# Kernel tuning notes

Hardware: AMD Instinct MI355X
Metric: run time of the kernel (lower is better)

## Reference

```python
import jax, jax.numpy as jnp
import numpy as np

N_NODES = 100000
N_EDGES = 3200000
F_IN = 512
F_OUT = 512
T_ITERS = 4
EPS = 1e-5


def setup_inputs() -> dict:
    key = jax.random.key(0)
    k1, k2, k3, k4, k5 = jax.random.split(key, 5)
    x = jax.random.normal(k1, (N_NODES, F_IN), dtype=jnp.float32)
    stdv = 1.0 / np.sqrt(F_OUT)
    weight = jax.random.uniform(k2, (F_IN, F_OUT), dtype=jnp.float32,
                                minval=-stdv, maxval=stdv)
    adj_rows = jax.random.randint(k3, (N_EDGES,), 0, N_NODES, dtype=jnp.int32)
    adj_cols = jax.random.randint(k4, (N_EDGES,), 0, N_NODES, dtype=jnp.int32)
    adj_vals = jax.random.uniform(k5, (N_EDGES,), dtype=jnp.float32)
    return {"x": x, "weight": weight, "adj_rows": adj_rows,
            "adj_cols": adj_cols, "adj_vals": adj_vals}


def oni_norm(weight):
    # norm_groups=1: Z is [in_features, out_features]
    Zc = weight - weight.mean(axis=-1, keepdims=True)
    S = Zc @ Zc.T + EPS * jnp.eye(Zc.shape[0], dtype=weight.dtype)
    norm_S = jnp.linalg.norm(S)  # Frobenius norm (scalar)
    S = S / norm_S
    B = jnp.eye(S.shape[-1], dtype=weight.dtype)
    for _ in range(T_ITERS):
        # baddbmm(1.5, B, -0.5, B^3, S) = 1.5*B - 0.5*(B@B@B)@S
        B3 = B @ B @ B
        B = 1.5 * B - 0.5 * (B3 @ S)
    W = (B @ Zc) / jnp.sqrt(norm_S)
    return W


def reference(x, weight, adj_rows, adj_cols, adj_vals):
    # Faithful to the torch forward: ONINorm(W) is computed (self.W) but the
    # dense mm uses the raw self.weight, exactly as in the source.
    W = oni_norm(weight)  # noqa: F841 (computed but unused, as in original)
    support = x @ weight                       # [N, F_OUT]
    # spmm: out[r] = sum_e adj_vals[e] * support[cols[e]] for rows[e] == r
    gathered = adj_vals[:, None] * support[adj_cols]  # [E, F_OUT]
    output = jax.ops.segment_sum(gathered, adj_rows, num_segments=N_NODES)
    return output
```

## Files before the change

kernel.cpp:

```cpp
#include <hip/hip_runtime.h>
#include <hip/hip_bf16.h>

#define N_NODESC 100000
#define N_EDGESC 3200000
#define FDIM 512
#define MPAD 100096
#define NBLK 256
#define EPB 12500
#define NBUCKB 391
#define NCNT (NBLK * NBUCKB)
#define NB_SCAN ((NCNT + 8191) / 8192)

typedef __attribute__((ext_vector_type(4))) float f32x4;
typedef __attribute__((ext_vector_type(8))) __bf16 bf16x8;
typedef __attribute__((ext_vector_type(4))) __bf16 bf16x4;
typedef unsigned long long u64;

__device__ __forceinline__ void gload_lds16(const void* g, void* l) {
  __builtin_amdgcn_global_load_lds(
      (const __attribute__((address_space(1))) unsigned int*)g,
      (__attribute__((address_space(3))) unsigned int*)l, 16, 0, 0);
}

__global__ void k_convert_wT(const float* __restrict__ w, __bf16* __restrict__ wT) {
  int i = blockIdx.x * 256 + threadIdx.x;
  if (i >= FDIM * FDIM) return;
  int k = i >> 9, n = i & (FDIM - 1);
  wT[n * FDIM + k] = (__bf16)w[i];
}

__global__ __launch_bounds__(256) void k_bcount(const int* __restrict__ rows,
                                                int* __restrict__ cnt) {
  __shared__ int h[NBUCKB];
  const int blk = blockIdx.x;
  for (int i = threadIdx.x; i < NBUCKB; i += 256) h[i] = 0;
  __syncthreads();
  const int e0 = blk * EPB;
  for (int e = e0 + threadIdx.x; e < e0 + EPB; e += 256)
    atomicAdd(&h[rows[e] >> 8], 1);
  __syncthreads();
  for (int i = threadIdx.x; i < NBUCKB; i += 256) cnt[i * NBLK + blk] = h[i];
}

__global__ __launch_bounds__(1024) void k_scan1(int* __restrict__ d, int* __restrict__ bsum) {
  __shared__ int s[1024];
  const int t = threadIdx.x;
  const int base = blockIdx.x * 8192 + t * 8;
  int v[8];
  int sum = 0;
  #pragma unroll
  for (int k = 0; k < 8; ++k) {
    v[k] = (base + k < NCNT) ? d[base + k] : 0;
    sum += v[k];
  }
  s[t] = sum;
  __syncthreads();
  for (int dl = 1; dl < 1024; dl <<= 1) {
    int a = s[t];
    int b = (t >= dl) ? s[t - dl] : 0;
    __syncthreads();
    s[t] = a + b;
    __syncthreads();
  }
  int excl = (t == 0) ? 0 : s[t - 1];
  #pragma unroll
  for (int k = 0; k < 8; ++k) {
    if (base + k < NCNT) d[base + k] = excl;
    excl += v[k];
  }
  if (t == 1023) bsum[blockIdx.x] = s[1023];
}

__global__ __launch_bounds__(1024) void k_scan2(int* __restrict__ bsum, int nb,
                                                int* __restrict__ d) {
  __shared__ int s[1024];
  const int t = threadIdx.x;
  s[t] = (t < nb) ? bsum[t] : 0;
  __syncthreads();
  for (int dl = 1; dl < 1024; dl <<= 1) {
    int a = s[t];
    int b = (t >= dl) ? s[t - dl] : 0;
    __syncthreads();
    s[t] = a + b;
    __syncthreads();
  }
  if (t < nb) bsum[t] = (t == 0) ? 0 : s[t - 1];
  if (t == 0) d[NCNT] = s[1023];
}

__global__ void k_scan3(int* __restrict__ d, const int* __restrict__ bsum) {
  int i = blockIdx.x * 256 + threadIdx.x;
  if (i >= NCNT) return;
  d[i] += bsum[i >> 13];
}

__global__ __launch_bounds__(256) void k_bscatter(const int* __restrict__ rows,
                                                  const int* __restrict__ cols,
                                                  const float* __restrict__ vals,
                                                  const int* __restrict__ off,
                                                  u64* __restrict__ bedges) {
  __shared__ int lofs[NBUCKB];
  __shared__ int lcur[NBUCKB];
  const int blk = blockIdx.x;
  for (int i = threadIdx.x; i < NBUCKB; i += 256) {
    lofs[i] = off[i * NBLK + blk];
    lcur[i] = 0;
  }
  __syncthreads();
  const int e0 = blk * EPB;
  for (int e = e0 + threadIdx.x; e < e0 + EPB; e += 256) {
    const int r = rows[e];
    const int b = r >> 8;
    const int p = lofs[b] + atomicAdd(&lcur[b], 1);
    bedges[p] = ((u64)__float_as_uint(vals[e]) << 32) |
                ((u64)(r & 255) << 17) | (unsigned)cols[e];
  }
}

__global__ __launch_bounds__(256) void k_csr(const int* __restrict__ off,
                                             const u64* __restrict__ bedges,
                                             u64* __restrict__ edges,
                                             int* __restrict__ row_off) {
  __shared__ int hcnt[256];
  __shared__ int hcur[256];
  const int b = blockIdx.x;
  const int t = threadIdx.x;
  const int base  = off[b * NBLK];
  const int nextb = (b + 1 < NBUCKB) ? off[(b + 1) * NBLK] : off[NCNT];
  hcnt[t] = 0;
  __syncthreads();
  for (int j = base + t; j < nextb; j += 256)
    atomicAdd(&hcnt[(int)(bedges[j] >> 17) & 255], 1);
  __syncthreads();
  for (int d = 1; d < 256; d <<= 1) {
    int a = hcnt[t];
    int u = (t >= d) ? hcnt[t - d] : 0;
    __syncthreads();
    hcnt[t] = a + u;
    __syncthreads();
  }
  const int excl = (t == 0) ? 0 : hcnt[t - 1];
  row_off[b * 256 + t] = base + excl;
  hcur[t] = base + excl;
  __syncthreads();
  for (int j = base + t; j < nextb; j += 256) {
    const u64 e = bedges[j];
    const int lr = (int)(e >> 17) & 255;
    const int p = atomicAdd(&hcur[lr], 1);
    edges[p] = (e & 0xFFFFFFFF00000000ull) | (e & 0x1FFFFull);
  }
}

__global__ __launch_bounds__(512) void k_gemm(const float* __restrict__ x,
                                              const __bf16* __restrict__ wT,
                                              __bf16* __restrict__ support) {
  __shared__ __bf16 lA[2][256 * 32];
  __shared__ __bf16 lB[2][256 * 32];
  const int tm = blockIdx.x >> 1;
  const int tn = blockIdx.x & 1;
  const int tid = threadIdx.x;
  const int wid = tid >> 6;
  const int lane = tid & 63;
  const int wm = wid >> 2;
  const int wn = wid & 3;

  const long rowA0 = (long)tm * 256;
  const int  ncol0 = tn * 256;

  const int srow  = lane >> 2;
  const int skoff = (lane & 3) * 8;

  const int arow = tid >> 1;
  const int ah   = (tid & 1) * 16;

  f32x4 acc[8][4];
  #pragma unroll
  for (int m = 0; m < 8; ++m)
    #pragma unroll
    for (int n = 0; n < 4; ++n)
      acc[m][n] = (f32x4){0.f, 0.f, 0.f, 0.f};

  const long grow = rowA0 + arow;
  const long arowc = (grow < N_NODESC) ? grow : (N_NODESC - 1);
  const bool apad = grow >= N_NODESC;

  float4 ar[4];
  auto issueA = [&](int kt) {
    const int k0 = kt * 32;
    #pragma unroll
    for (int i = 0; i < 4; ++i)
      ar[i] = *(const float4*)(x + arowc * FDIM + k0 + ah + 4 * i);
  };
  auto writeA = [&](int buf) {
    #pragma unroll
    for (int i = 0; i < 4; ++i) {
      bf16x4 o;
      o[0] = (__bf16)(apad ? 0.f : ar[i].x);
      o[1] = (__bf16)(apad ? 0.f : ar[i].y);
      o[2] = (__bf16)(apad ? 0.f : ar[i].z);
      o[3] = (__bf16)(apad ? 0.f : ar[i].w);
      *(bf16x4*)&lA[buf][arow * 32 + ah + 4 * i] = o;
    }
  };
  auto stageB = [&](int buf, int kt) {
    const int k0 = kt * 32;
    #pragma unroll
    for (int it = 0; it < 2; ++it) {
      const int c = wid * 2 + it;
      const __bf16* gB = wT + (long)(ncol0 + c * 16 + srow) * FDIM + k0 + skoff;
      gload_lds16(gB, &lB[buf][c * 512]);
    }
  };

  issueA(0);
  stageB(0, 0);
  writeA(0);
  __syncthreads();

  const int frow = lane & 15;
  const int fk   = (lane >> 4) * 8;

  for (int kt = 0; kt < 16; ++kt) {
    const int buf = kt & 1;
    if (kt < 15) {
      issueA(kt + 1);
      stageB(buf ^ 1, kt + 1);
    }
    bf16x8 a[8], b[4];
    #pragma unroll
    for (int m = 0; m < 8; ++m)
      a[m] = *(const bf16x8*)&lA[buf][(wm * 128 + m * 16 + frow) * 32 + fk];
    #pragma unroll
    for (int n = 0; n < 4; ++n)
      b[n] = *(const bf16x8*)&lB[buf][(wn * 64 + n * 16 + frow) * 32 + fk];
    #pragma unroll
    for (int m = 0; m < 8; ++m)
      #pragma unroll
      for (int n = 0; n < 4; ++n)
        acc[m][n] = __builtin_amdgcn_mfma_f32_16x16x32_bf16(a[m], b[n], acc[m][n], 0, 0, 0);
    if (kt < 15) writeA(buf ^ 1);
    __syncthreads();
  }

  const long crow0 = (long)tm * 256 + wm * 128 + (lane >> 4) * 4;
  const int  ccol0 = tn * 256 + wn * 64 + frow;
  #pragma unroll
  for (int m = 0; m < 8; ++m)
    #pragma unroll
    for (int n = 0; n < 4; ++n)
      #pragma unroll
      for (int i = 0; i < 4; ++i)
        support[(crow0 + m * 16 + i) * (long)FDIM + ccol0 + n * 16] = (__bf16)acc[m][n][i];
}

__global__ __launch_bounds__(256) void k_spmm(const int* __restrict__ row_off,
                                              const u64* __restrict__ edges,
                                              const __bf16* __restrict__ support,
                                              float* __restrict__ out) {
  const int r = blockIdx.x * 4 + (threadIdx.x >> 6);
  const int lane = threadIdx.x & 63;
  if (r >= N_NODESC) return;
  const int beg = row_off[r];
  const int end = row_off[r + 1];
  const __bf16* sp = support + lane * 8;

  float acc[8];
  #pragma unroll
  for (int i = 0; i < 8; ++i) acc[i] = 0.f;

  int j = beg;
  for (; j + 1 < end; j += 2) {
    const u64 e0 = edges[j];
    const u64 e1 = edges[j + 1];
    const bf16x8 s0 = *(const bf16x8*)(sp + (long)(unsigned)(e0 & 0xffffffffu) * FDIM);
    const bf16x8 s1 = *(const bf16x8*)(sp + (long)(unsigned)(e1 & 0xffffffffu) * FDIM);
    const float v0 = __uint_as_float((unsigned)(e0 >> 32));
    const float v1 = __uint_as_float((unsigned)(e1 >> 32));
    #pragma unroll
    for (int i = 0; i < 8; ++i) acc[i] += v0 * (float)s0[i];
    #pragma unroll
    for (int i = 0; i < 8; ++i) acc[i] += v1 * (float)s1[i];
  }
  if (j < end) {
    const u64 e0 = edges[j];
    const bf16x8 s0 = *(const bf16x8*)(sp + (long)(unsigned)(e0 & 0xffffffffu) * FDIM);
    const float v0 = __uint_as_float((unsigned)(e0 >> 32));
    #pragma unroll
    for (int i = 0; i < 8; ++i) acc[i] += v0 * (float)s0[i];
  }

  *(float4*)(out + (long)r * FDIM + lane * 8) =
      make_float4(acc[0], acc[1], acc[2], acc[3]);
  *(float4*)(out + (long)r * FDIM + lane * 8 + 4) =
      make_float4(acc[4], acc[5], acc[6], acc[7]);
}

extern "C" void kernel_launch(void* const* d_in, const int* in_sizes, int n_in,
                              void* d_out, int out_size, void* d_ws, size_t ws_size,
                              hipStream_t stream) {
  const float* x    = (const float*)d_in[0];
  const float* w    = (const float*)d_in[1];
  const int*   rows = (const int*)d_in[2];
  const int*   cols = (const int*)d_in[3];
  const float* vals = (const float*)d_in[4];
  float* out = (float*)d_out;

  char* ws = (char*)d_ws;
  size_t off = 0;
  auto alloc = [&](size_t bytes) {
    void* p = ws + off;
    off += (bytes + 255) & ~(size_t)255;
    return p;
  };
  __bf16* support = (__bf16*)alloc((size_t)MPAD * FDIM * 2);
  __bf16* wT      = (__bf16*)alloc((size_t)FDIM * FDIM * 2);
  int*    cnt     = (int*)alloc((size_t)(NCNT + 1) * 4);
  int*    row_off = (int*)alloc((size_t)(MPAD + 1) * 4);
  int*    bsum    = (int*)alloc(1024 * 4);
  u64*    edges   = (u64*)alloc((size_t)N_EDGESC * 8);
  u64*    bedges  = (u64*)alloc((size_t)N_EDGESC * 8);
  (void)ws_size;

  k_convert_wT<<<(FDIM * FDIM + 255) / 256, 256, 0, stream>>>(w, wT);
  k_bcount<<<NBLK, 256, 0, stream>>>(rows, cnt);
  k_scan1<<<NB_SCAN, 1024, 0, stream>>>(cnt, bsum);
  k_scan2<<<1, 1024, 0, stream>>>(bsum, NB_SCAN, cnt);
  k_scan3<<<(NCNT + 255) / 256, 256, 0, stream>>>(cnt, bsum);
  k_bscatter<<<NBLK, 256, 0, stream>>>(rows, cols, vals, cnt, bedges);
  k_csr<<<NBUCKB, 256, 0, stream>>>(cnt, bedges, edges, row_off);
  k_gemm<<<(MPAD / 256) * 2, 512, 0, stream>>>(x, wT, support);
  k_spmm<<<N_NODESC / 4, 256, 0, stream>>>(row_off, edges, support, out);
}
```

Before: 745.8 us.

## Use full-width 128x512 GEMM tiles and fuse weight transpose into bucket count

The GEMM now has each block compute a 128-row by full 512-column tile, where before two blocks each computed a 256x256 half. Each x row is therefore read from global memory and converted to bf16 once instead of twice, at the cost of staging all of W per k-step and changing the LDS footprint and per-wave tile shape. The weight transpose/convert kernel is merged into the bucket-count kernel as extra blocks, which removes one launch.

```diff
diff --git a/kernel.cpp b/kernel.cpp
--- a/kernel.cpp
+++ b/kernel.cpp
@@ -13,7 +13,6 @@
 
 typedef __attribute__((ext_vector_type(4))) float f32x4;
 typedef __attribute__((ext_vector_type(8))) __bf16 bf16x8;
-typedef __attribute__((ext_vector_type(4))) __bf16 bf16x4;
 typedef unsigned long long u64;
 
 __device__ __forceinline__ void gload_lds16(const void* g, void* l) {
@@ -22,16 +21,22 @@
       (__attribute__((address_space(3))) unsigned int*)l, 16, 0, 0);
 }
 
-__global__ void k_convert_wT(const float* __restrict__ w, __bf16* __restrict__ wT) {
-  int i = blockIdx.x * 256 + threadIdx.x;
-  if (i >= FDIM * FDIM) return;
-  int k = i >> 9, n = i & (FDIM - 1);
-  wT[n * FDIM + k] = (__bf16)w[i];
-}
-
-__global__ __launch_bounds__(256) void k_bcount(const int* __restrict__ rows,
-                                                int* __restrict__ cnt) {
+__global__ __launch_bounds__(256) void k_bcount_wt(const int* __restrict__ rows,
+                                                   int* __restrict__ cnt,
+                                                   const float* __restrict__ w,
+                                                   __bf16* __restrict__ wT) {
   __shared__ int h[NBUCKB];
+  if (blockIdx.x >= NBLK) {
+    const int b = blockIdx.x - NBLK;
+    const int i0 = b * 1024 + threadIdx.x * 4;
+    #pragma unroll
+    for (int q = 0; q < 4; ++q) {
+      const int j = i0 + q;
+      const int k = j >> 9, n = j & (FDIM - 1);
+      wT[n * FDIM + k] = (__bf16)w[j];
+    }
+    return;
+  }
   const int blk = blockIdx.x;
   for (int i = threadIdx.x; i < NBUCKB; i += 256) h[i] = 0;
   __syncthreads();
@@ -154,60 +159,58 @@
 __global__ __launch_bounds__(512) void k_gemm(const float* __restrict__ x,
                                               const __bf16* __restrict__ wT,
                                               __bf16* __restrict__ support) {
-  __shared__ __bf16 lA[2][256 * 32];
-  __shared__ __bf16 lB[2][256 * 32];
-  const int tm = blockIdx.x >> 1;
-  const int tn = blockIdx.x & 1;
+  __shared__ __bf16 lA[2][128 * 32];
+  __shared__ __bf16 lB[2][512 * 32];
+  const int tm = blockIdx.x;
   const int tid = threadIdx.x;
   const int wid = tid >> 6;
   const int lane = tid & 63;
   const int wm = wid >> 2;
   const int wn = wid & 3;
 
-  const long rowA0 = (long)tm * 256;
-  const int  ncol0 = tn * 256;
+  const long rowA0 = (long)tm * 128;
 
   const int srow  = lane >> 2;
   const int skoff = (lane & 3) * 8;
 
-  const int arow = tid >> 1;
-  const int ah   = (tid & 1) * 16;
-
-  f32x4 acc[8][4];
-  #pragma unroll
-  for (int m = 0; m < 8; ++m)
-    #pragma unroll
-    for (int n = 0; n < 4; ++n)
+  const int arow = tid >> 2;
+  const int ah   = (tid & 3) * 8;
+
+  f32x4 acc[4][8];
+  #pragma unroll
+  for (int m = 0; m < 4; ++m)
+    #pragma unroll
+    for (int n = 0; n < 8; ++n)
       acc[m][n] = (f32x4){0.f, 0.f, 0.f, 0.f};
 
   const long grow = rowA0 + arow;
   const long arowc = (grow < N_NODESC) ? grow : (N_NODESC - 1);
   const bool apad = grow >= N_NODESC;
 
-  float4 ar[4];
+  float4 ar[2];
   auto issueA = [&](int kt) {
     const int k0 = kt * 32;
-    #pragma unroll
-    for (int i = 0; i < 4; ++i)
-      ar[i] = *(const float4*)(x + arowc * FDIM + k0 + ah + 4 * i);
+    ar[0] = *(const float4*)(x + arowc * FDIM + k0 + ah);
+    ar[1] = *(const float4*)(x + arowc * FDIM + k0 + ah + 4);
   };
   auto writeA = [&](int buf) {
-    #pragma unroll
-    for (int i = 0; i < 4; ++i) {
-      bf16x4 o;
-      o[0] = (__bf16)(apad ? 0.f : ar[i].x);
-      o[1] = (__bf16)(apad ? 0.f : ar[i].y);
-      o[2] = (__bf16)(apad ? 0.f : ar[i].z);
-      o[3] = (__bf16)(apad ? 0.f : ar[i].w);
-      *(bf16x4*)&lA[buf][arow * 32 + ah + 4 * i] = o;
-    }
+    bf16x8 o;
+    o[0] = (__bf16)(apad ? 0.f : ar[0].x);
+    o[1] = (__bf16)(apad ? 0.f : ar[0].y);
+    o[2] = (__bf16)(apad ? 0.f : ar[0].z);
+    o[3] = (__bf16)(apad ? 0.f : ar[0].w);
+    o[4] = (__bf16)(apad ? 0.f : ar[1].x);
+    o[5] = (__bf16)(apad ? 0.f : ar[1].y);
+    o[6] = (__bf16)(apad ? 0.f : ar[1].z);
+    o[7] = (__bf16)(apad ? 0.f : ar[1].w);
+    *(bf16x8*)&lA[buf][arow * 32 + ah] = o;
   };
   auto stageB = [&](int buf, int kt) {
     const int k0 = kt * 32;
     #pragma unroll
-    for (int it = 0; it < 2; ++it) {
-      const int c = wid * 2 + it;
-      const __bf16* gB = wT + (long)(ncol0 + c * 16 + srow) * FDIM + k0 + skoff;
+    for (int it = 0; it < 4; ++it) {
+      const int c = wid * 4 + it;
+      const __bf16* gB = wT + (long)(c * 16 + srow) * FDIM + k0 + skoff;
       gload_lds16(gB, &lB[buf][c * 512]);
     }
   };
@@ -226,28 +229,28 @@
       issueA(kt + 1);
       stageB(buf ^ 1, kt + 1);
     }
-    bf16x8 a[8], b[4];
-    #pragma unroll
-    for (int m = 0; m < 8; ++m)
-      a[m] = *(const bf16x8*)&lA[buf][(wm * 128 + m * 16 + frow) * 32 + fk];
-    #pragma unroll
-    for (int n = 0; n < 4; ++n)
-      b[n] = *(const bf16x8*)&lB[buf][(wn * 64 + n * 16 + frow) * 32 + fk];
-    #pragma unroll
-    for (int m = 0; m < 8; ++m)
+    bf16x8 a[4], b[8];
+    #pragma unroll
+    for (int m = 0; m < 4; ++m)
+      a[m] = *(const bf16x8*)&lA[buf][(wm * 64 + m * 16 + frow) * 32 + fk];
+    #pragma unroll
+    for (int n = 0; n < 8; ++n)
+      b[n] = *(const bf16x8*)&lB[buf][(wn * 128 + n * 16 + frow) * 32 + fk];
+    #pragma unroll
+    for (int m = 0; m < 4; ++m)
       #pragma unroll
-      for (int n = 0; n < 4; ++n)
+      for (int n = 0; n < 8; ++n)
         acc[m][n] = __builtin_amdgcn_mfma_f32_16x16x32_bf16(a[m], b[n], acc[m][n], 0, 0, 0);
     if (kt < 15) writeA(buf ^ 1);
     __syncthreads();
   }
 
-  const long crow0 = (long)tm * 256 + wm * 128 + (lane >> 4) * 4;
-  const int  ccol0 = tn * 256 + wn * 64 + frow;
-  #pragma unroll
-  for (int m = 0; m < 8; ++m)
-    #pragma unroll
-    for (int n = 0; n < 4; ++n)
+  const long crow0 = (long)tm * 128 + wm * 64 + (lane >> 4) * 4;
+  const int  ccol0 = wn * 128 + frow;
+  #pragma unroll
+  for (int m = 0; m < 4; ++m)
+    #pragma unroll
+    for (int n = 0; n < 8; ++n)
       #pragma unroll
       for (int i = 0; i < 4; ++i)
         support[(crow0 + m * 16 + i) * (long)FDIM + ccol0 + n * 16] = (__bf16)acc[m][n][i];
@@ -321,13 +324,12 @@
   u64*    bedges  = (u64*)alloc((size_t)N_EDGESC * 8);
   (void)ws_size;
 
-  k_convert_wT<<<(FDIM * FDIM + 255) / 256, 256, 0, stream>>>(w, wT);
-  k_bcount<<<NBLK, 256, 0, stream>>>(rows, cnt);
+  k_bcount_wt<<<NBLK + 256, 256, 0, stream>>>(rows, cnt, w, wT);
   k_scan1<<<NB_SCAN, 1024, 0, stream>>>(cnt, bsum);
   k_scan2<<<1, 1024, 0, stream>>>(bsum, NB_SCAN, cnt);
   k_scan3<<<(NCNT + 255) / 256, 256, 0, stream>>>(cnt, bsum);
   k_bscatter<<<NBLK, 256, 0, stream>>>(rows, cols, vals, cnt, bedges);
   k_csr<<<NBUCKB, 256, 0, stream>>>(cnt, bedges, edges, row_off);
-  k_gemm<<<(MPAD / 256) * 2, 512, 0, stream>>>(x, wT, support);
+  k_gemm<<<MPAD / 128, 512, 0, stream>>>(x, wT, support);
   k_spmm<<<N_NODESC / 4, 256, 0, stream>>>(row_off, edges, support, out);
 }
```

New measurement: 720.3 us. 3.4% less time.
